# Optimization experiments

Hardware: AMD Instinct MI355X
Metric: run time of the kernel (lower is better)

The kernel has to match this reference:

```python
import jax, jax.numpy as jnp
import numpy as np

N_T, N_S, F_IN, H, N_OUT = 2048, 512, 7, 64, 3


def setup_inputs() -> dict:
    key = jax.random.key(0)
    ks = jax.random.split(key, 12)
    pts = jax.random.normal(ks[0], (N_T, 3), jnp.float32)
    centers = jax.random.normal(ks[1], (N_S, 3), jnp.float32)
    nrm = jax.random.normal(ks[2], (N_S, 3), jnp.float32)
    normals = nrm / jnp.linalg.norm(nrm, axis=-1, keepdims=True)
    areas = jax.random.uniform(ks[3], (N_S,), jnp.float32, 0.1, 1.0)
    ref_lengths = jax.random.uniform(ks[4], (2,), jnp.float32, 0.5, 1.5)

    def lin(k, i, o):
        return jax.random.normal(k, (i, o), jnp.float32) / np.float32(np.sqrt(i))

    return {
        "prediction_points": pts,
        "face_centers": centers,
        "face_normals": normals,
        "face_areas": areas,
        "reference_lengths": ref_lengths,
        "W1": lin(ks[5], F_IN, H), "b1": jnp.zeros((H,), jnp.float32),
        "W2": lin(ks[6], H, H),    "b2": jnp.zeros((H,), jnp.float32),
        "W3": lin(ks[7], H, H),    "b3": jnp.zeros((H,), jnp.float32),
        "Wout": lin(ks[8], H, N_OUT), "bout": jnp.zeros((N_OUT,), jnp.float32),
        "p_scale": jnp.float32(1.0), "p_bias": jnp.float32(0.0),
        "v_scale": jnp.float32(1.0), "v_bias": jnp.float32(0.0),
    }


def reference(prediction_points, face_centers, face_normals, face_areas,
              reference_lengths, W1, b1, W2, b2, W3, b3, Wout, bout,
              p_scale, p_bias, v_scale, v_bias):
    eps = jnp.float32(1e-8)
    # Pairwise relative geometry (translation/rotation-equivariant features).
    rvec = prediction_points[:, None, :] - face_centers[None, :, :]  # [T,S,3]
    r2 = jnp.sum(rvec * rvec, axis=-1)                               # [T,S]
    r = jnp.sqrt(r2 + eps)
    rhat = rvec / r[..., None]
    c = jnp.sum(rhat * face_normals[None, :, :], axis=-1)            # cos(angle)
    # Legendre polynomials P0..P3 (n_spherical_harmonics = 4).
    legendre = jnp.stack(
        [jnp.ones_like(c), c, 0.5 * (3.0 * c * c - 1.0),
         0.5 * (5.0 * c * c * c - 3.0 * c)], axis=-1)                # [T,S,4]
    # Multiscale nondimensional distance features, one per reference length.
    dfeat = 1.0 / (1.0 + r[..., None] / reference_lengths)           # [T,S,2]
    afeat = jnp.broadcast_to(jnp.log(face_areas)[None, :, None],
                             r.shape + (1,))                          # [T,S,1]
    feats = jnp.concatenate([dfeat, legendre, afeat], axis=-1)       # [T,S,7]
    # Kernel MLP evaluated per (target, source) pair.
    h = jnp.tanh(feats @ W1 + b1)
    h = jnp.tanh(h @ W2 + b2)
    h = jnp.tanh(h @ W3 + b3)
    out = h @ Wout + bout                                            # [T,S,3]
    # Green's-function-like decay, area-weighted boundary integral.
    decay = face_areas[None, :] / (r2 + 1.0)                         # [T,S]
    p = jnp.sum(out[..., 0] * decay, axis=1)                         # [T]
    vel = jnp.sum((out[..., 1:2] * rhat
                   + out[..., 2:3] * face_normals[None, :, :])
                  * decay[..., None], axis=1)                        # [T,3]
    pressure = p * p_scale + p_bias
    velocity = vel * v_scale + v_bias
    return jnp.concatenate([pressure[:, None], velocity], axis=-1)   # [T,4]
```

## Files before the change

kernel.cpp:

```cpp
#include <hip/hip_runtime.h>
#include <hip/hip_fp16.h>


#define N_T 2048
#define N_S 512
#define BLK 128
#define SCALE 2.885390081777927f

#define CPY_F 5888
#define CPY_U 1472

typedef _Float16 f16;
typedef _Float16 f16x4 __attribute__((ext_vector_type(4)));
typedef float f32x4 __attribute__((ext_vector_type(4)));
typedef unsigned short u16;
typedef unsigned int u32;

__device__ __forceinline__ float tanh_s(float x) {
    float e = __builtin_amdgcn_exp2f(x);
    return fmaf(-2.0f, __builtin_amdgcn_rcpf(e + 1.0f), 1.0f);
}

__device__ __forceinline__ f32x4 mfma16(f16x4 a, f16x4 b, f32x4 c) {
    return __builtin_amdgcn_mfma_f32_16x16x16f16(a, b, c, 0, 0, 0);
}

__device__ __forceinline__ u32 pkrtz(float a, float b) {
    return __builtin_bit_cast(u32, __builtin_amdgcn_cvt_pkrtz(a, b));
}

__device__ __forceinline__ f16x4 lo4(uint4 g) {
    uint2 p; p.x = g.x; p.y = g.y;
    return __builtin_bit_cast(f16x4, p);
}
__device__ __forceinline__ f16x4 hi4(uint4 g) {
    uint2 p; p.x = g.z; p.y = g.w;
    return __builtin_bit_cast(f16x4, p);
}

__device__ __forceinline__ f16x4 tpack(f32x4 c) {
    uint2 p;
    p.x = pkrtz(tanh_s(c[0]), tanh_s(c[1]));
    p.y = pkrtz(tanh_s(c[2]), tanh_s(c[3]));
    return __builtin_bit_cast(f16x4, p);
}

__global__ __launch_bounds__(256) void prep_kernel(
    const float* __restrict__ W1, const float* __restrict__ b1,
    const float* __restrict__ W2, const float* __restrict__ b2,
    const float* __restrict__ W3, const float* __restrict__ b3,
    const float* __restrict__ Wout, float* __restrict__ ws)
{
    const int tid = blockIdx.x * 256 + threadIdx.x;
    if (tid < 5632) {
        const int cpy = tid / 1408;
        const int r   = tid - cpy * 1408;
        const int u   = r >> 6, lane = r & 63;
        const int q = lane >> 4, l15 = lane & 15;
        float x[8];
        bool lo = false;
        #pragma unroll
        for (int e = 0; e < 8; ++e) {
            const int half = e >> 2, j = e & 3;
            float v;
            if (u < 2) {
                const int mt = u * 2 + half;
                const int k = q * 4 + j;
                v = (k < 7) ? W1[k * 64 + mt * 16 + l15] * SCALE : 0.f;
            } else if (u < 10) {
                const int idx = u - 2, mt = idx >> 1, kp = idx & 1;
                const int k = (kp * 2 + half) * 16 + q * 4 + j;
                v = W2[k * 64 + mt * 16 + l15] * SCALE;
            } else if (u < 18) {
                const int idx = u - 10, mt = idx >> 1, kp = idx & 1;
                const int k = (kp * 2 + half) * 16 + q * 4 + j;
                v = W3[k * 64 + mt * 16 + l15] * SCALE;
            } else {
                const int kp = (u - 18) & 1;
                const int k = (kp * 2 + half) * 16 + q * 4 + j;
                v = (l15 < 3) ? Wout[k * 3 + l15] : 0.f;
                lo = (u >= 20);
            }
            x[e] = v;
        }
        u16 outw[8];
        #pragma unroll
        for (int e = 0; e < 8; ++e) {
            const f16 h = (f16)x[e];
            const f16 val = lo ? (f16)(x[e] - (float)h) : h;
            outw[e] = __builtin_bit_cast(u16, val);
        }
        uint4 g;
        g.x = outw[0] | ((u32)outw[1] << 16);
        g.y = outw[2] | ((u32)outw[3] << 16);
        g.z = outw[4] | ((u32)outw[5] << 16);
        g.w = outw[6] | ((u32)outw[7] << 16);
        *(uint4*)((char*)ws + (size_t)cpy * CPY_F * 4 + (size_t)(u * 64 + lane) * 16) = g;
    } else {
        const int b = tid - 5632;
        const int cpy = b / 192, i = b - cpy * 192;
        const int Lb = i >> 6, j = i & 63;
        float bv;
        if (Lb == 0)      bv = b1[j];
        else if (Lb == 1) bv = b2[j];
        else              bv = b3[j];
        ws[cpy * CPY_F + 5632 + i] = bv * SCALE;
    }
}

__global__ __launch_bounds__(BLK, 2) void globe_mfma(
    const float* __restrict__ pts, const float* __restrict__ ctr,
    const float* __restrict__ nrm, const float* __restrict__ areas,
    const float* __restrict__ rlen, const float* __restrict__ bout,
    const float* __restrict__ p_scale, const float* __restrict__ p_bias,
    const float* __restrict__ v_scale, const float* __restrict__ v_bias,
    const float* __restrict__ ws,
    float* __restrict__ out)
{
    __shared__ __align__(16) u16 featL[2][2][64][8];
    __shared__ __align__(16) uint4 geomL[2][2][64];
    __shared__ float xr[4];

    const int tid  = threadIdx.x;
    const int lane = tid & 63;
    const int wv   = tid >> 6;
    const int l15  = lane & 15;
    const int q    = lane >> 4;
    const int qf   = q & 1;
    const int t    = blockIdx.x;

    const float px = pts[3 * t + 0], py = pts[3 * t + 1], pz = pts[3 * t + 2];
    const float invL0 = __builtin_amdgcn_rcpf(rlen[0]);
    const float invL1 = __builtin_amdgcn_rcpf(rlen[1]);
    f32x4 co_init = (f32x4){0.f, 0.f, 0.f, 0.f};
    if (q == 0) { co_init[0] = bout[0]; co_init[1] = bout[1]; co_init[2] = bout[2]; }

    const f16x4 bz = (f16x4){0, 0, 0, 0};
    float accp = 0.f, avx = 0.f, avy = 0.f, avz = 0.f;

    #pragma unroll 1
    for (int ch = 0; ch < 2; ++ch) {
        const uint4* __restrict__ wsU = (const uint4*)ws + (ch * 2) * CPY_U;
        const float* __restrict__ wsBias = ws + (ch * 2) * CPY_F + 5632;

        #pragma unroll
        for (int st = 0; st < 2; ++st) {
            const int s = (wv * 4 + ch * 2 + st) * 64 + lane;
            const float cx = ctr[3 * s + 0], cy = ctr[3 * s + 1], cz = ctr[3 * s + 2];
            const float snx = nrm[3 * s + 0], sny = nrm[3 * s + 1], snz = nrm[3 * s + 2];
            const float ar = areas[s];
            const float rvx = px - cx, rvy = py - cy, rvz = pz - cz;
            const float r2 = rvx * rvx + rvy * rvy + rvz * rvz;
            const float r2e = r2 + 1e-8f;
            const float rinv = __builtin_amdgcn_rsqf(r2e);
            const float r = r2e * rinv;
            const float rhx = rvx * rinv, rhy = rvy * rinv, rhz = rvz * rinv;
            const float cth = rhx * snx + rhy * sny + rhz * snz;
            const float c2 = cth * cth;
            const float decay = ar * __builtin_amdgcn_rcpf(r2 + 1.0f);
            uint4 fw;
            fw.x = pkrtz(__builtin_amdgcn_rcpf(fmaf(r, invL0, 1.0f)),
                         __builtin_amdgcn_rcpf(fmaf(r, invL1, 1.0f)));
            fw.y = pkrtz(1.0f, cth);
            fw.z = pkrtz(fmaf(1.5f, c2, -0.5f), cth * fmaf(2.5f, c2, -1.5f));
            fw.w = pkrtz(__logf(ar), 0.0f);
            *(uint4*)&featL[wv][st][lane][0] = fw;
            uint4 g;
            g.x = __builtin_bit_cast(u32, decay);
            g.y = pkrtz(rhx, rhy);
            g.z = pkrtz(rhz, snx);
            g.w = pkrtz(sny, snz);
            geomL[wv][st][lane] = g;
        }

        f16x4 B2[2][4][4];
        {
            const uint4 g0 = wsU[0 * 64 + lane], g1 = wsU[1 * 64 + lane];
            f16x4 a1[4];
            a1[0] = lo4(g0); a1[1] = hi4(g0); a1[2] = lo4(g1); a1[3] = hi4(g1);
            float4 bv[4];
            #pragma unroll
            for (int mt = 0; mt < 4; ++mt)
                bv[mt] = *(const float4*)(wsBias + 0 * 64 + mt * 16 + q * 4);
            #pragma unroll
            for (int n4 = 0; n4 < 4; ++n4) {
                f16x4 bf[2];
                #pragma unroll
                for (int st = 0; st < 2; ++st) {
                    const f16x4 lv = *(const f16x4*)&featL[wv][st][n4 * 16 + l15][qf * 4];
                    bf[st] = (q < 2) ? lv : bz;
                }
                f32x4 c[2][4];
                #pragma unroll
                for (int mt = 0; mt < 4; ++mt) {
                    c[0][mt] = (f32x4){bv[mt].x, bv[mt].y, bv[mt].z, bv[mt].w};
                    c[1][mt] = c[0][mt];
                    c[0][mt] = mfma16(a1[mt], bf[0], c[0][mt]);
                    c[1][mt] = mfma16(a1[mt], bf[1], c[1][mt]);
                }
                #pragma unroll
                for (int mt = 0; mt < 4; ++mt) {
                    B2[0][mt][n4] = tpack(c[0][mt]);
                    B2[1][mt][n4] = tpack(c[1][mt]);
                }
            }
        }

        f16x4 B3[2][4][4];
        {
            f16x4 a[4][4];
            #pragma unroll
            for (int mt = 0; mt < 4; ++mt) {
                const uint4 ga = wsU[(2 + 2 * mt) * 64 + lane];
                const uint4 gb = wsU[(3 + 2 * mt) * 64 + lane];
                a[mt][0] = lo4(ga); a[mt][1] = hi4(ga);
                a[mt][2] = lo4(gb); a[mt][3] = hi4(gb);
            }
            float4 bv[4];
            #pragma unroll
            for (int mt = 0; mt < 4; ++mt)
                bv[mt] = *(const float4*)(wsBias + 1 * 64 + mt * 16 + q * 4);
            #pragma unroll
            for (int n4 = 0; n4 < 4; ++n4) {
                f32x4 c[2][4];
                #pragma unroll
                for (int mt = 0; mt < 4; ++mt) {
                    c[0][mt] = (f32x4){bv[mt].x, bv[mt].y, bv[mt].z, bv[mt].w};
                    c[1][mt] = c[0][mt];
                }
                #pragma unroll
                for (int kt = 0; kt < 4; ++kt)
                    #pragma unroll
                    for (int mt = 0; mt < 4; ++mt) {
                        c[0][mt] = mfma16(a[mt][kt], B2[0][kt][n4], c[0][mt]);
                        c[1][mt] = mfma16(a[mt][kt], B2[1][kt][n4], c[1][mt]);
                    }
                #pragma unroll
                for (int mt = 0; mt < 4; ++mt) {
                    B3[0][mt][n4] = tpack(c[0][mt]);
                    B3[1][mt][n4] = tpack(c[1][mt]);
                }
            }
        }

        f16x4 BO[2][4][4];
        {
            f16x4 a[4][4];
            #pragma unroll
            for (int mt = 0; mt < 4; ++mt) {
                const uint4 ga = wsU[(10 + 2 * mt) * 64 + lane];
                const uint4 gb = wsU[(11 + 2 * mt) * 64 + lane];
                a[mt][0] = lo4(ga); a[mt][1] = hi4(ga);
                a[mt][2] = lo4(gb); a[mt][3] = hi4(gb);
            }
            float4 bv[4];
            #pragma unroll
            for (int mt = 0; mt < 4; ++mt)
                bv[mt] = *(const float4*)(wsBias + 2 * 64 + mt * 16 + q * 4);
            #pragma unroll
            for (int n4 = 0; n4 < 4; ++n4) {
                f32x4 c[2][4];
                #pragma unroll
                for (int mt = 0; mt < 4; ++mt) {
                    c[0][mt] = (f32x4){bv[mt].x, bv[mt].y, bv[mt].z, bv[mt].w};
                    c[1][mt] = c[0][mt];
                }
                #pragma unroll
                for (int kt = 0; kt < 4; ++kt)
                    #pragma unroll
                    for (int mt = 0; mt < 4; ++mt) {
                        c[0][mt] = mfma16(a[mt][kt], B3[0][kt][n4], c[0][mt]);
                        c[1][mt] = mfma16(a[mt][kt], B3[1][kt][n4], c[1][mt]);
                    }
                #pragma unroll
                for (int mt = 0; mt < 4; ++mt) {
                    BO[0][mt][n4] = tpack(c[0][mt]);
                    BO[1][mt][n4] = tpack(c[1][mt]);
                }
            }
        }

        {
            const uint4 gh0 = wsU[18 * 64 + lane], gh1 = wsU[19 * 64 + lane];
            const uint4 gl0 = wsU[20 * 64 + lane], gl1 = wsU[21 * 64 + lane];
            f16x4 aoh[4], aol[4];
            aoh[0] = lo4(gh0); aoh[1] = hi4(gh0); aoh[2] = lo4(gh1); aoh[3] = hi4(gh1);
            aol[0] = lo4(gl0); aol[1] = hi4(gl0); aol[2] = lo4(gl1); aol[3] = hi4(gl1);
            #pragma unroll
            for (int n4 = 0; n4 < 4; ++n4) {
                f32x4 co[2];
                co[0] = co_init; co[1] = co_init;
                #pragma unroll
                for (int kt = 0; kt < 4; ++kt) {
                    co[0] = mfma16(aoh[kt], BO[0][kt][n4], co[0]);
                    co[1] = mfma16(aoh[kt], BO[1][kt][n4], co[1]);
                    co[0] = mfma16(aol[kt], BO[0][kt][n4], co[0]);
                    co[1] = mfma16(aol[kt], BO[1][kt][n4], co[1]);
                }
                if (q == 0) {
                    #pragma unroll
                    for (int st = 0; st < 2; ++st) {
                        const uint4 g = geomL[wv][st][n4 * 16 + l15];
                        const float d = __builtin_bit_cast(float, g.x);
                        const float2 rxy = __half22float2(__builtin_bit_cast(__half2, g.y));
                        const float2 rzx = __half22float2(__builtin_bit_cast(__half2, g.z));
                        const float2 nyz = __half22float2(__builtin_bit_cast(__half2, g.w));
                        const float o0 = co[st][0], o1 = co[st][1], o2 = co[st][2];
                        accp = fmaf(o0, d, accp);
                        avx  = fmaf(fmaf(o1, rxy.x, o2 * rzx.y), d, avx);
                        avy  = fmaf(fmaf(o1, rxy.y, o2 * nyz.x), d, avy);
                        avz  = fmaf(fmaf(o1, rzx.x, o2 * nyz.y), d, avz);
                    }
                }
            }
        }
    }

    #pragma unroll
    for (int off = 8; off > 0; off >>= 1) {
        accp += __shfl_down(accp, off);
        avx  += __shfl_down(avx,  off);
        avy  += __shfl_down(avy,  off);
        avz  += __shfl_down(avz,  off);
    }

    if (wv == 1 && lane == 0) {
        xr[0] = accp; xr[1] = avx; xr[2] = avy; xr[3] = avz;
    }
    __syncthreads();
    if (wv == 0 && lane == 0) {
        accp += xr[0]; avx += xr[1]; avy += xr[2]; avz += xr[3];
        const float ps = p_scale[0], pb = p_bias[0];
        const float vs = v_scale[0], vb = v_bias[0];
        out[4 * t + 0] = fmaf(accp, ps, pb);
        out[4 * t + 1] = fmaf(avx, vs, vb);
        out[4 * t + 2] = fmaf(avy, vs, vb);
        out[4 * t + 3] = fmaf(avz, vs, vb);
    }
}

extern "C" void kernel_launch(void* const* d_in, const int* in_sizes, int n_in,
                              void* d_out, int out_size, void* d_ws, size_t ws_size,
                              hipStream_t stream) {
    (void)in_sizes; (void)n_in; (void)ws_size; (void)out_size;
    const float* pts   = (const float*)d_in[0];
    const float* ctr   = (const float*)d_in[1];
    const float* nrm   = (const float*)d_in[2];
    const float* areas = (const float*)d_in[3];
    const float* rlen  = (const float*)d_in[4];
    const float* W1    = (const float*)d_in[5];
    const float* b1    = (const float*)d_in[6];
    const float* W2    = (const float*)d_in[7];
    const float* b2    = (const float*)d_in[8];
    const float* W3    = (const float*)d_in[9];
    const float* b3    = (const float*)d_in[10];
    const float* Wout  = (const float*)d_in[11];
    const float* bout  = (const float*)d_in[12];
    const float* ps    = (const float*)d_in[13];
    const float* pb    = (const float*)d_in[14];
    const float* vs    = (const float*)d_in[15];
    const float* vb    = (const float*)d_in[16];
    float* ws = (float*)d_ws;

    prep_kernel<<<25, 256, 0, stream>>>(W1, b1, W2, b2, W3, b3, Wout, ws);
    globe_mfma<<<N_T, BLK, 0, stream>>>(
        pts, ctr, nrm, areas, rlen, bout, ps, pb, vs, vb, ws, (float*)d_out);
}
```

Measured before the change: 144.9 us.

## Use 16x16x32 f16 MFMA and batch tanh reciprocals across four values

Replaces pairs of 16x16x16 MFMAs with single 16x16x32 MFMAs (available on gfx950), repacking activations into f16x8 fragments so the K dimension is consumed in two steps instead of four. The tanh is also rewritten to share one reciprocal across four elements via product tricks, with the exp input clamped to avoid overflow. This halves MFMA instruction count and cuts the transcendental reciprocal count, at the cost of extra multiplies and slightly different rounding. The K-index mapping of the combined fragments must match the pre-packed weight layout for correctness.

```diff
diff --git a/kernel.cpp b/kernel.cpp
--- a/kernel.cpp
+++ b/kernel.cpp
@@ -12,17 +12,16 @@
 
 typedef _Float16 f16;
 typedef _Float16 f16x4 __attribute__((ext_vector_type(4)));
+typedef _Float16 f16x8 __attribute__((ext_vector_type(8)));
 typedef float f32x4 __attribute__((ext_vector_type(4)));
 typedef unsigned short u16;
 typedef unsigned int u32;
 
-__device__ __forceinline__ float tanh_s(float x) {
-    float e = __builtin_amdgcn_exp2f(x);
-    return fmaf(-2.0f, __builtin_amdgcn_rcpf(e + 1.0f), 1.0f);
-}
-
 __device__ __forceinline__ f32x4 mfma16(f16x4 a, f16x4 b, f32x4 c) {
     return __builtin_amdgcn_mfma_f32_16x16x16f16(a, b, c, 0, 0, 0);
+}
+__device__ __forceinline__ f32x4 mfma32(f16x8 a, f16x8 b, f32x4 c) {
+    return __builtin_amdgcn_mfma_f32_16x16x32_f16(a, b, c, 0, 0, 0);
 }
 
 __device__ __forceinline__ u32 pkrtz(float a, float b) {
@@ -37,11 +36,28 @@
     uint2 p; p.x = g.z; p.y = g.w;
     return __builtin_bit_cast(f16x4, p);
 }
+__device__ __forceinline__ f16x8 all8(uint4 g) {
+    return __builtin_bit_cast(f16x8, g);
+}
+__device__ __forceinline__ f16x8 cat8(f16x4 a, f16x4 b) {
+    return __builtin_shufflevector(a, b, 0, 1, 2, 3, 4, 5, 6, 7);
+}
 
 __device__ __forceinline__ f16x4 tpack(f32x4 c) {
+    const float a0 = __builtin_amdgcn_exp2f(fminf(c[0], 30.f)) + 1.f;
+    const float a1 = __builtin_amdgcn_exp2f(fminf(c[1], 30.f)) + 1.f;
+    const float a2 = __builtin_amdgcn_exp2f(fminf(c[2], 30.f)) + 1.f;
+    const float a3 = __builtin_amdgcn_exp2f(fminf(c[3], 30.f)) + 1.f;
+    const float p01 = a0 * a1, p23 = a2 * a3;
+    const float r = __builtin_amdgcn_rcpf(p01 * p23);
+    const float r01 = r * p23, r23 = r * p01;
+    const float t0 = fmaf(-2.f, r01 * a1, 1.f);
+    const float t1 = fmaf(-2.f, r01 * a0, 1.f);
+    const float t2 = fmaf(-2.f, r23 * a3, 1.f);
+    const float t3 = fmaf(-2.f, r23 * a2, 1.f);
     uint2 p;
-    p.x = pkrtz(tanh_s(c[0]), tanh_s(c[1]));
-    p.y = pkrtz(tanh_s(c[2]), tanh_s(c[3]));
+    p.x = pkrtz(t0, t1);
+    p.y = pkrtz(t2, t3);
     return __builtin_bit_cast(f16x4, p);
 }
 
@@ -173,7 +189,7 @@
             geomL[wv][st][lane] = g;
         }
 
-        f16x4 B2[2][4][4];
+        f16x8 B2[2][2][4];
         {
             const uint4 g0 = wsU[0 * 64 + lane], g1 = wsU[1 * 64 + lane];
             f16x4 a1[4];
@@ -199,22 +215,20 @@
                     c[1][mt] = mfma16(a1[mt], bf[1], c[1][mt]);
                 }
                 #pragma unroll
-                for (int mt = 0; mt < 4; ++mt) {
-                    B2[0][mt][n4] = tpack(c[0][mt]);
-                    B2[1][mt][n4] = tpack(c[1][mt]);
-                }
-            }
-        }
-
-        f16x4 B3[2][4][4];
+                for (int kk = 0; kk < 2; ++kk) {
+                    B2[0][kk][n4] = cat8(tpack(c[0][2 * kk]), tpack(c[0][2 * kk + 1]));
+                    B2[1][kk][n4] = cat8(tpack(c[1][2 * kk]), tpack(c[1][2 * kk + 1]));
+                }
+            }
+        }
+
+        f16x8 B3[2][2][4];
         {
-            f16x4 a[4][4];
+            f16x8 a[4][2];
             #pragma unroll
             for (int mt = 0; mt < 4; ++mt) {
-                const uint4 ga = wsU[(2 + 2 * mt) * 64 + lane];
-                const uint4 gb = wsU[(3 + 2 * mt) * 64 + lane];
-                a[mt][0] = lo4(ga); a[mt][1] = hi4(ga);
-                a[mt][2] = lo4(gb); a[mt][3] = hi4(gb);
+                a[mt][0] = all8(wsU[(2 + 2 * mt) * 64 + lane]);
+                a[mt][1] = all8(wsU[(3 + 2 * mt) * 64 + lane]);
             }
             float4 bv[4];
             #pragma unroll
@@ -229,29 +243,27 @@
                     c[1][mt] = c[0][mt];
                 }
                 #pragma unroll
-                for (int kt = 0; kt < 4; ++kt)
+                for (int kk = 0; kk < 2; ++kk)
                     #pragma unroll
                     for (int mt = 0; mt < 4; ++mt) {
-                        c[0][mt] = mfma16(a[mt][kt], B2[0][kt][n4], c[0][mt]);
-                        c[1][mt] = mfma16(a[mt][kt], B2[1][kt][n4], c[1][mt]);
+                        c[0][mt] = mfma32(a[mt][kk], B2[0][kk][n4], c[0][mt]);
+                        c[1][mt] = mfma32(a[mt][kk], B2[1][kk][n4], c[1][mt]);
                     }
                 #pragma unroll
-                for (int mt = 0; mt < 4; ++mt) {
-                    B3[0][mt][n4] = tpack(c[0][mt]);
-                    B3[1][mt][n4] = tpack(c[1][mt]);
-                }
-            }
-        }
-
-        f16x4 BO[2][4][4];
+                for (int kk = 0; kk < 2; ++kk) {
+                    B3[0][kk][n4] = cat8(tpack(c[0][2 * kk]), tpack(c[0][2 * kk + 1]));
+                    B3[1][kk][n4] = cat8(tpack(c[1][2 * kk]), tpack(c[1][2 * kk + 1]));
+                }
+            }
+        }
+
+        f16x8 BO[2][2][4];
         {
-            f16x4 a[4][4];
+            f16x8 a[4][2];
             #pragma unroll
             for (int mt = 0; mt < 4; ++mt) {
-                const uint4 ga = wsU[(10 + 2 * mt) * 64 + lane];
-                const uint4 gb = wsU[(11 + 2 * mt) * 64 + lane];
-                a[mt][0] = lo4(ga); a[mt][1] = hi4(ga);
-                a[mt][2] = lo4(gb); a[mt][3] = hi4(gb);
+                a[mt][0] = all8(wsU[(10 + 2 * mt) * 64 + lane]);
+                a[mt][1] = all8(wsU[(11 + 2 * mt) * 64 + lane]);
             }
             float4 bv[4];
             #pragma unroll
@@ -266,37 +278,37 @@
                     c[1][mt] = c[0][mt];
                 }
                 #pragma unroll
-                for (int kt = 0; kt < 4; ++kt)
+                for (int kk = 0; kk < 2; ++kk)
                     #pragma unroll
                     for (int mt = 0; mt < 4; ++mt) {
-                        c[0][mt] = mfma16(a[mt][kt], B3[0][kt][n4], c[0][mt]);
-                        c[1][mt] = mfma16(a[mt][kt], B3[1][kt][n4], c[1][mt]);
+                        c[0][mt] = mfma32(a[mt][kk], B3[0][kk][n4], c[0][mt]);
+                        c[1][mt] = mfma32(a[mt][kk], B3[1][kk][n4], c[1][mt]);
                     }
                 #pragma unroll
-                for (int mt = 0; mt < 4; ++mt) {
-                    BO[0][mt][n4] = tpack(c[0][mt]);
-                    BO[1][mt][n4] = tpack(c[1][mt]);
+                for (int kk = 0; kk < 2; ++kk) {
+                    BO[0][kk][n4] = cat8(tpack(c[0][2 * kk]), tpack(c[0][2 * kk + 1]));
+                    BO[1][kk][n4] = cat8(tpack(c[1][2 * kk]), tpack(c[1][2 * kk + 1]));
                 }
             }
         }
 
         {
-            const uint4 gh0 = wsU[18 * 64 + lane], gh1 = wsU[19 * 64 + lane];
-            const uint4 gl0 = wsU[20 * 64 + lane], gl1 = wsU[21 * 64 + lane];
-            f16x4 aoh[4], aol[4];
-            aoh[0] = lo4(gh0); aoh[1] = hi4(gh0); aoh[2] = lo4(gh1); aoh[3] = hi4(gh1);
-            aol[0] = lo4(gl0); aol[1] = hi4(gl0); aol[2] = lo4(gl1); aol[3] = hi4(gl1);
+            const f16x8 aoh0 = all8(wsU[18 * 64 + lane]);
+            const f16x8 aoh1 = all8(wsU[19 * 64 + lane]);
+            const f16x8 aol0 = all8(wsU[20 * 64 + lane]);
+            const f16x8 aol1 = all8(wsU[21 * 64 + lane]);
             #pragma unroll
             for (int n4 = 0; n4 < 4; ++n4) {
                 f32x4 co[2];
                 co[0] = co_init; co[1] = co_init;
-                #pragma unroll
-                for (int kt = 0; kt < 4; ++kt) {
-                    co[0] = mfma16(aoh[kt], BO[0][kt][n4], co[0]);
-                    co[1] = mfma16(aoh[kt], BO[1][kt][n4], co[1]);
-                    co[0] = mfma16(aol[kt], BO[0][kt][n4], co[0]);
-                    co[1] = mfma16(aol[kt], BO[1][kt][n4], co[1]);
-                }
+                co[0] = mfma32(aoh0, BO[0][0][n4], co[0]);
+                co[1] = mfma32(aoh0, BO[1][0][n4], co[1]);
+                co[0] = mfma32(aol0, BO[0][0][n4], co[0]);
+                co[1] = mfma32(aol0, BO[1][0][n4], co[1]);
+                co[0] = mfma32(aoh1, BO[0][1][n4], co[0]);
+                co[1] = mfma32(aoh1, BO[1][1][n4], co[1]);
+                co[0] = mfma32(aol1, BO[0][1][n4], co[0]);
+                co[1] = mfma32(aol1, BO[1][1][n4], co[1]);
                 if (q == 0) {
                     #pragma unroll
                     for (int st = 0; st < 2; ++st) {
```

After: 161.2 us. 11.2% more time.
